# Optimization experiments

Measured on AMD Instinct MI355X. Metric: run time of the kernel, lower is better.

Reference implementation:

```python
import jax, jax.numpy as jnp
import numpy as np

H = 4096      # hidden_size (also vocab size of the embedding, per source)
O = 4096      # output_size (also embedding dim, per source)
MAX_LEN = 15


def setup_inputs() -> dict:
    key = jax.random.key(0)
    ks = jax.random.split(key, 16)
    s = 0.02  # init scale
    inp = {
        "input_ids": jax.random.randint(ks[0], (1,), 0, H),
        "hidden": jax.random.normal(ks[1], (1, 1, H), jnp.float32),
        "e_output": jax.random.normal(ks[2], (1, H), jnp.float32),   # unused, kept for signature fidelity
        "e_output_seq": jax.random.normal(ks[3], (MAX_LEN, H), jnp.float32),
        # parameters
        "emb_W": jax.random.normal(ks[4], (H, O), jnp.float32) * s,
        "att_W": jax.random.normal(ks[5], (MAX_LEN, H + O), jnp.float32) * s,
        "att_b": jnp.zeros((MAX_LEN,), jnp.float32),
        "comb_W": jax.random.normal(ks[6], (H, H + O), jnp.float32) * s,
        "comb_b": jnp.zeros((H,), jnp.float32),
        "gru_W_ih": jax.random.normal(ks[7], (3 * H, H), jnp.float32) * s,
        "gru_W_hh": jax.random.normal(ks[8], (3 * H, H), jnp.float32) * s,
        "gru_b_ih": jnp.zeros((3 * H,), jnp.float32),
        "gru_b_hh": jnp.zeros((3 * H,), jnp.float32),
        "out_W": jax.random.normal(ks[9], (O, H), jnp.float32) * s,
        "out_b": jnp.zeros((O,), jnp.float32),
    }
    return inp


def reference(input_ids, hidden, e_output, e_output_seq, emb_W, att_W, att_b,
              comb_W, comb_b, gru_W_ih, gru_W_hh, gru_b_ih, gru_b_hh, out_W, out_b):
    # dropout is identity in eval mode
    emb = emb_W[input_ids[0]][None, :]                       # [1, O]
    h0 = hidden[0]                                            # [1, H]
    att_logits = jnp.concatenate([emb, h0], axis=1) @ att_W.T + att_b
    att_weights = jax.nn.softmax(att_logits, axis=-1)         # [1, MAX_LEN]
    att_applied = att_weights @ e_output_seq                   # [1, H]
    combined = jnp.concatenate([emb, att_applied], axis=1)     # [1, H+O]
    x = jax.nn.relu(combined @ comb_W.T + comb_b)              # [1, H]
    # GRU cell (PyTorch gate order: r, z, n)
    gi = x @ gru_W_ih.T + gru_b_ih                             # [1, 3H]
    gh = h0 @ gru_W_hh.T + gru_b_hh                            # [1, 3H]
    i_r, i_z, i_n = jnp.split(gi, 3, axis=1)
    h_r, h_z, h_n = jnp.split(gh, 3, axis=1)
    r = jax.nn.sigmoid(i_r + h_r)
    z = jax.nn.sigmoid(i_z + h_z)
    n = jnp.tanh(i_n + r * h_n)
    h_new = (1.0 - z) * n + z * h0                             # [1, H]
    out = jax.nn.log_softmax(h_new @ out_W.T + out_b, axis=-1)  # [1, O]
    return out, h_new[None, :, :], att_weights
```

## Files before the change

### kernel.cpp

```cpp
#include <hip/hip_runtime.h>

#define H 4096
#define O 4096
#define HO 8192
#define MAXLEN 15

__device__ __forceinline__ float wave_dot(const float* __restrict__ w,
                                          const float* __restrict__ x,
                                          int K, int lane) {
    const float4* w4 = (const float4*)w;
    const float4* x4 = (const float4*)x;
    float acc = 0.f;
    int n4 = K >> 2;
    for (int i = lane; i < n4; i += 64) {
        float4 wv = w4[i];
        float4 xv = x4[i];
        acc += wv.x * xv.x + wv.y * xv.y + wv.z * xv.z + wv.w * xv.w;
    }
    #pragma unroll
    for (int off = 32; off; off >>= 1) acc += __shfl_down(acc, off, 64);
    return acc;
}

__global__ void k_att(const int* __restrict__ ids,
                      const float* __restrict__ hidden,
                      const float* __restrict__ eseq,
                      const float* __restrict__ embW,
                      const float* __restrict__ attW,
                      const float* __restrict__ attb,
                      float* __restrict__ combined,
                      float* __restrict__ out_attw) {
    __shared__ float s_logit[MAXLEN];
    __shared__ float s_w[MAXLEN];
    const int tid  = threadIdx.x;
    const int wave = tid >> 6, lane = tid & 63;
    const int id = ids[0];
    const float* emb = embW + (size_t)id * O;

    for (int k = tid; k < O; k += blockDim.x) combined[k] = emb[k];

    if (wave < MAXLEN) {
        const float* wrow = attW + (size_t)wave * (H + O);
        float acc = 0.f;
        for (int t = lane; t < O; t += 64) acc += emb[t] * wrow[t];
        for (int t = lane; t < H; t += 64) acc += hidden[t] * wrow[O + t];
        #pragma unroll
        for (int off = 32; off; off >>= 1) acc += __shfl_down(acc, off, 64);
        if (lane == 0) s_logit[wave] = acc + attb[wave];
    }
    __syncthreads();
    if (tid == 0) {
        float m = -1e30f;
        for (int j = 0; j < MAXLEN; j++) m = fmaxf(m, s_logit[j]);
        float s = 0.f;
        for (int j = 0; j < MAXLEN; j++) { float e = __expf(s_logit[j] - m); s_w[j] = e; s += e; }
        float inv = 1.f / s;
        for (int j = 0; j < MAXLEN; j++) { s_w[j] *= inv; out_attw[j] = s_w[j]; }
    }
    __syncthreads();
    for (int k = tid; k < H; k += blockDim.x) {
        float acc = 0.f;
        #pragma unroll
        for (int j = 0; j < MAXLEN; j++) acc += s_w[j] * eseq[j * H + k];
        combined[O + k] = acc;
    }
}

__global__ void k_comb_ghh(const float* __restrict__ combW,
                           const float* __restrict__ combB,
                           const float* __restrict__ ghhW,
                           const float* __restrict__ ghhB,
                           const float* __restrict__ hidden,
                           const float* __restrict__ combined,
                           float* __restrict__ xout,
                           float* __restrict__ ghout) {
    const int wave = threadIdx.x >> 6, lane = threadIdx.x & 63;
    const int b = blockIdx.x;
    if (b < 1024) {
        int row = b * 4 + wave;
        float d = wave_dot(combW + (size_t)row * HO, combined, HO, lane);
        if (lane == 0) xout[row] = fmaxf(d + combB[row], 0.f);
    } else {
        int row = (b - 1024) * 4 + wave;
        float d = wave_dot(ghhW + (size_t)row * H, hidden, H, lane);
        if (lane == 0) ghout[row] = d + ghhB[row];
    }
}

__global__ void k_gru(const float* __restrict__ gihW,
                      const float* __restrict__ gihB,
                      const float* __restrict__ hidden,
                      const float* __restrict__ x,
                      const float* __restrict__ gh,
                      float* __restrict__ hout,
                      float* __restrict__ out_h) {
    const int wave = threadIdx.x >> 6, lane = threadIdx.x & 63;
    const int i = blockIdx.x * 4 + wave;
    float d0 = wave_dot(gihW + (size_t)i * H,           x, H, lane);
    float d1 = wave_dot(gihW + (size_t)(i + H) * H,     x, H, lane);
    float d2 = wave_dot(gihW + (size_t)(i + 2 * H) * H, x, H, lane);
    if (lane == 0) {
        float ir = d0 + gihB[i];
        float iz = d1 + gihB[i + H];
        float in_ = d2 + gihB[i + 2 * H];
        float hr = gh[i], hz = gh[i + H], hn = gh[i + 2 * H];
        float r = 1.f / (1.f + __expf(-(ir + hr)));
        float z = 1.f / (1.f + __expf(-(iz + hz)));
        float n = tanhf(in_ + r * hn);
        float h0 = hidden[i];
        float h = (1.f - z) * n + z * h0;
        hout[i] = h;
        out_h[i] = h;
    }
}

__global__ void k_out(const float* __restrict__ outW,
                      const float* __restrict__ outB,
                      const float* __restrict__ h,
                      float* __restrict__ logits) {
    const int wave = threadIdx.x >> 6, lane = threadIdx.x & 63;
    const int i = blockIdx.x * 4 + wave;
    float d = wave_dot(outW + (size_t)i * H, h, H, lane);
    if (lane == 0) logits[i] = d + outB[i];
}

__global__ void k_lsm(const float* __restrict__ logits, float* __restrict__ out) {
    __shared__ float red[16];
    __shared__ float red2[16];
    const int tid = threadIdx.x, lane = tid & 63, wave = tid >> 6;
    float m = -1e30f;
    for (int k = tid; k < O; k += 1024) m = fmaxf(m, logits[k]);
    #pragma unroll
    for (int off = 32; off; off >>= 1) m = fmaxf(m, __shfl_down(m, off, 64));
    if (lane == 0) red[wave] = m;
    __syncthreads();
    if (tid == 0) {
        float mm = -1e30f;
        for (int j = 0; j < 16; j++) mm = fmaxf(mm, red[j]);
        red[0] = mm;
    }
    __syncthreads();
    m = red[0];
    float s = 0.f;
    for (int k = tid; k < O; k += 1024) s += __expf(logits[k] - m);
    #pragma unroll
    for (int off = 32; off; off >>= 1) s += __shfl_down(s, off, 64);
    if (lane == 0) red2[wave] = s;
    __syncthreads();
    if (tid == 0) {
        float ss = 0.f;
        for (int j = 0; j < 16; j++) ss += red2[j];
        red2[0] = m + logf(ss);
    }
    __syncthreads();
    float lse = red2[0];
    for (int k = tid; k < O; k += 1024) out[k] = logits[k] - lse;
}

extern "C" void kernel_launch(void* const* d_in, const int* in_sizes, int n_in,
                              void* d_out, int out_size, void* d_ws, size_t ws_size,
                              hipStream_t stream) {
    const int*   ids    = (const int*)d_in[0];
    const float* hidden = (const float*)d_in[1];
    const float* eseq   = (const float*)d_in[3];
    const float* embW   = (const float*)d_in[4];
    const float* attW   = (const float*)d_in[5];
    const float* attb   = (const float*)d_in[6];
    const float* combW  = (const float*)d_in[7];
    const float* combB  = (const float*)d_in[8];
    const float* gihW   = (const float*)d_in[9];
    const float* ghhW   = (const float*)d_in[10];
    const float* gihB   = (const float*)d_in[11];
    const float* ghhB   = (const float*)d_in[12];
    const float* outW   = (const float*)d_in[13];
    const float* outB   = (const float*)d_in[14];
    float* out = (float*)d_out;

    float* ws       = (float*)d_ws;
    float* combined = ws;
    float* xbuf     = ws + 8192;
    float* ghbuf    = ws + 12288;
    float* hbuf     = ws + 24576;
    float* logits   = ws + 28672;

    k_att     <<<1,    960,  0, stream>>>(ids, hidden, eseq, embW, attW, attb, combined, out + 8192);
    k_comb_ghh<<<4096, 256,  0, stream>>>(combW, combB, ghhW, ghhB, hidden, combined, xbuf, ghbuf);
    k_gru     <<<1024, 256,  0, stream>>>(gihW, gihB, hidden, xbuf, ghbuf, hbuf, out + 4096);
    k_out     <<<1024, 256,  0, stream>>>(outW, outB, hbuf, logits);
    k_lsm     <<<1,    1024, 0, stream>>>(logits, out);
}
```

Baseline: 614.4 us.

## Fuse decoder step into one persistent kernel with grid barriers

```diff
diff --git a/kernel.cpp b/kernel.cpp
--- a/kernel.cpp
+++ b/kernel.cpp
@@ -4,188 +4,229 @@
 #define O 4096
 #define HO 8192
 #define MAXLEN 15
-
-__device__ __forceinline__ float wave_dot(const float* __restrict__ w,
-                                          const float* __restrict__ x,
-                                          int K, int lane) {
-    const float4* w4 = (const float4*)w;
+#define NBLK 512
+
+struct Args {
+    const int* ids;
+    const float* hidden;
+    const float* eseq;
+    const float* embW;
+    const float* attW;
+    const float* attb;
+    const float* combW;
+    const float* combB;
+    const float* gihW;
+    const float* gihB;
+    const float* ghhW;
+    const float* ghhB;
+    const float* outW;
+    const float* outB;
+    float* out;
+    float* ws;
+};
+
+__device__ __forceinline__ float dot4f(const float4 a, const float4 b) {
+    return a.x * b.x + a.y * b.y + a.z * b.z + a.w * b.w;
+}
+
+#define XRED(v) { _Pragma("unroll") for (int o_ = 32; o_; o_ >>= 1) v += __shfl_xor(v, o_, 64); }
+
+__device__ __forceinline__ void loadx16(const float* __restrict__ x, int lane, float4 xs[16]) {
     const float4* x4 = (const float4*)x;
-    float acc = 0.f;
-    int n4 = K >> 2;
-    for (int i = lane; i < n4; i += 64) {
-        float4 wv = w4[i];
-        float4 xv = x4[i];
-        acc += wv.x * xv.x + wv.y * xv.y + wv.z * xv.z + wv.w * xv.w;
-    }
     #pragma unroll
-    for (int off = 32; off; off >>= 1) acc += __shfl_down(acc, off, 64);
-    return acc;
-}
-
-__global__ void k_att(const int* __restrict__ ids,
-                      const float* __restrict__ hidden,
-                      const float* __restrict__ eseq,
-                      const float* __restrict__ embW,
-                      const float* __restrict__ attW,
-                      const float* __restrict__ attb,
-                      float* __restrict__ combined,
-                      float* __restrict__ out_attw) {
-    __shared__ float s_logit[MAXLEN];
-    __shared__ float s_w[MAXLEN];
-    const int tid  = threadIdx.x;
-    const int wave = tid >> 6, lane = tid & 63;
-    const int id = ids[0];
-    const float* emb = embW + (size_t)id * O;
-
-    for (int k = tid; k < O; k += blockDim.x) combined[k] = emb[k];
-
-    if (wave < MAXLEN) {
-        const float* wrow = attW + (size_t)wave * (H + O);
-        float acc = 0.f;
-        for (int t = lane; t < O; t += 64) acc += emb[t] * wrow[t];
-        for (int t = lane; t < H; t += 64) acc += hidden[t] * wrow[O + t];
-        #pragma unroll
-        for (int off = 32; off; off >>= 1) acc += __shfl_down(acc, off, 64);
-        if (lane == 0) s_logit[wave] = acc + attb[wave];
-    }
+    for (int c = 0; c < 16; c++) xs[c] = x4[lane + c * 64];
+}
+
+__device__ __forceinline__ void dot16x2(const float* __restrict__ w0,
+                                        const float* __restrict__ w1,
+                                        const float4 xs[16], int lane,
+                                        float& s0, float& s1) {
+    const float4* a4 = (const float4*)w0;
+    const float4* b4 = (const float4*)w1;
+    float x0 = 0.f, x1 = 0.f;
+    #pragma unroll
+    for (int c = 0; c < 16; c++) {
+        x0 += dot4f(a4[lane + c * 64], xs[c]);
+        x1 += dot4f(b4[lane + c * 64], xs[c]);
+    }
+    s0 += x0; s1 += x1;
+}
+
+__device__ __forceinline__ void gsync(unsigned* ctr) {
     __syncthreads();
-    if (tid == 0) {
+    if (threadIdx.x == 0) {
+        __threadfence();
+        __hip_atomic_fetch_add(ctr, 1u, __ATOMIC_ACQ_REL, __HIP_MEMORY_SCOPE_AGENT);
+        while (__hip_atomic_load(ctr, __ATOMIC_ACQUIRE, __HIP_MEMORY_SCOPE_AGENT) < NBLK)
+            __builtin_amdgcn_s_sleep(2);
+        __threadfence();
+    }
+    __syncthreads();
+}
+
+__global__ void k_zero(unsigned* c) { if (threadIdx.x < 16) c[threadIdx.x] = 0; }
+
+__global__ __launch_bounds__(256, 2) void k_fused(Args a) {
+    __shared__ float red[4];
+    __shared__ float red2[4];
+    unsigned* ctr   = (unsigned*)a.ws;
+    float* combined = a.ws + 64;
+    float* xbuf     = a.ws + 64 + 8192;
+    float* hbuf     = a.ws + 64 + 12288;
+    float* logits   = a.ws + 64 + 16384;
+    float* attlog   = a.ws + 64 + 20480;
+
+    const int tid = threadIdx.x, lane = tid & 63, w4 = tid >> 6;
+    const int gw = blockIdx.x * 4 + w4;
+    const int i0 = gw, i1 = gw + 2048;
+
+    float hr0, hz0, hn0, hr1, hz1, hn1;
+    {
+        float4 hs[16];
+        loadx16(a.hidden, lane, hs);
+        float s00 = 0.f, s10 = 0.f, s01 = 0.f, s11 = 0.f, s02 = 0.f, s12 = 0.f;
+        dot16x2(a.ghhW + (size_t)i0 * H,           a.ghhW + (size_t)i1 * H,           hs, lane, s00, s10);
+        dot16x2(a.ghhW + (size_t)(i0 + H) * H,     a.ghhW + (size_t)(i1 + H) * H,     hs, lane, s01, s11);
+        dot16x2(a.ghhW + (size_t)(i0 + 2 * H) * H, a.ghhW + (size_t)(i1 + 2 * H) * H, hs, lane, s02, s12);
+        XRED(s00); XRED(s10); XRED(s01); XRED(s11); XRED(s02); XRED(s12);
+        hr0 = s00 + a.ghhB[i0]; hz0 = s01 + a.ghhB[i0 + H]; hn0 = s02 + a.ghhB[i0 + 2 * H];
+        hr1 = s10 + a.ghhB[i1]; hz1 = s11 + a.ghhB[i1 + H]; hn1 = s12 + a.ghhB[i1 + 2 * H];
+
+        if (gw < MAXLEN) {
+            const int id = a.ids[0];
+            const float* ar = a.attW + (size_t)gw * HO;
+            float4 es[16];
+            loadx16(a.embW + (size_t)id * O, lane, es);
+            float sa = 0.f, sb = 0.f;
+            dot16x2(ar, ar + O, es, lane, sa, sb);
+            sb = 0.f;
+            {
+                const float4* b4 = (const float4*)(ar + O);
+                #pragma unroll
+                for (int c = 0; c < 16; c++) sb += dot4f(b4[lane + c * 64], hs[c]);
+            }
+            float s = sa + sb;
+            XRED(s);
+            if (lane == 0) attlog[gw] = s + a.attb[gw];
+        }
+    }
+    gsync(ctr + 0);
+
+    if (blockIdx.x < 32) {
+        const int k = blockIdx.x * 256 + tid;
+        float l[MAXLEN];
         float m = -1e30f;
-        for (int j = 0; j < MAXLEN; j++) m = fmaxf(m, s_logit[j]);
+        #pragma unroll
+        for (int j = 0; j < MAXLEN; j++) { l[j] = attlog[j]; m = fmaxf(m, l[j]); }
         float s = 0.f;
-        for (int j = 0; j < MAXLEN; j++) { float e = __expf(s_logit[j] - m); s_w[j] = e; s += e; }
-        float inv = 1.f / s;
-        for (int j = 0; j < MAXLEN; j++) { s_w[j] *= inv; out_attw[j] = s_w[j]; }
-    }
-    __syncthreads();
-    for (int k = tid; k < H; k += blockDim.x) {
-        float acc = 0.f;
-        #pragma unroll
-        for (int j = 0; j < MAXLEN; j++) acc += s_w[j] * eseq[j * H + k];
-        combined[O + k] = acc;
-    }
-}
-
-__global__ void k_comb_ghh(const float* __restrict__ combW,
-                           const float* __restrict__ combB,
-                           const float* __restrict__ ghhW,
-                           const float* __restrict__ ghhB,
-                           const float* __restrict__ hidden,
-                           const float* __restrict__ combined,
-                           float* __restrict__ xout,
-                           float* __restrict__ ghout) {
-    const int wave = threadIdx.x >> 6, lane = threadIdx.x & 63;
-    const int b = blockIdx.x;
-    if (b < 1024) {
-        int row = b * 4 + wave;
-        float d = wave_dot(combW + (size_t)row * HO, combined, HO, lane);
-        if (lane == 0) xout[row] = fmaxf(d + combB[row], 0.f);
-    } else {
-        int row = (b - 1024) * 4 + wave;
-        float d = wave_dot(ghhW + (size_t)row * H, hidden, H, lane);
-        if (lane == 0) ghout[row] = d + ghhB[row];
-    }
-}
-
-__global__ void k_gru(const float* __restrict__ gihW,
-                      const float* __restrict__ gihB,
-                      const float* __restrict__ hidden,
-                      const float* __restrict__ x,
-                      const float* __restrict__ gh,
-                      float* __restrict__ hout,
-                      float* __restrict__ out_h) {
-    const int wave = threadIdx.x >> 6, lane = threadIdx.x & 63;
-    const int i = blockIdx.x * 4 + wave;
-    float d0 = wave_dot(gihW + (size_t)i * H,           x, H, lane);
-    float d1 = wave_dot(gihW + (size_t)(i + H) * H,     x, H, lane);
-    float d2 = wave_dot(gihW + (size_t)(i + 2 * H) * H, x, H, lane);
-    if (lane == 0) {
-        float ir = d0 + gihB[i];
-        float iz = d1 + gihB[i + H];
-        float in_ = d2 + gihB[i + 2 * H];
-        float hr = gh[i], hz = gh[i + H], hn = gh[i + 2 * H];
-        float r = 1.f / (1.f + __expf(-(ir + hr)));
-        float z = 1.f / (1.f + __expf(-(iz + hz)));
-        float n = tanhf(in_ + r * hn);
-        float h0 = hidden[i];
-        float h = (1.f - z) * n + z * h0;
-        hout[i] = h;
-        out_h[i] = h;
-    }
-}
-
-__global__ void k_out(const float* __restrict__ outW,
-                      const float* __restrict__ outB,
-                      const float* __restrict__ h,
-                      float* __restrict__ logits) {
-    const int wave = threadIdx.x >> 6, lane = threadIdx.x & 63;
-    const int i = blockIdx.x * 4 + wave;
-    float d = wave_dot(outW + (size_t)i * H, h, H, lane);
-    if (lane == 0) logits[i] = d + outB[i];
-}
-
-__global__ void k_lsm(const float* __restrict__ logits, float* __restrict__ out) {
-    __shared__ float red[16];
-    __shared__ float red2[16];
-    const int tid = threadIdx.x, lane = tid & 63, wave = tid >> 6;
-    float m = -1e30f;
-    for (int k = tid; k < O; k += 1024) m = fmaxf(m, logits[k]);
-    #pragma unroll
-    for (int off = 32; off; off >>= 1) m = fmaxf(m, __shfl_down(m, off, 64));
-    if (lane == 0) red[wave] = m;
-    __syncthreads();
-    if (tid == 0) {
-        float mm = -1e30f;
-        for (int j = 0; j < 16; j++) mm = fmaxf(mm, red[j]);
-        red[0] = mm;
-    }
-    __syncthreads();
-    m = red[0];
-    float s = 0.f;
-    for (int k = tid; k < O; k += 1024) s += __expf(logits[k] - m);
-    #pragma unroll
-    for (int off = 32; off; off >>= 1) s += __shfl_down(s, off, 64);
-    if (lane == 0) red2[wave] = s;
-    __syncthreads();
-    if (tid == 0) {
-        float ss = 0.f;
-        for (int j = 0; j < 16; j++) ss += red2[j];
-        red2[0] = m + logf(ss);
-    }
-    __syncthreads();
-    float lse = red2[0];
-    for (int k = tid; k < O; k += 1024) out[k] = logits[k] - lse;
+        #pragma unroll
+        for (int j = 0; j < MAXLEN; j++) { l[j] = __expf(l[j] - m); s += l[j]; }
+        const float inv = 1.f / s;
+        if (k < O) {
+            combined[k] = a.embW[(size_t)a.ids[0] * O + k];
+            if (k < MAXLEN) a.out[8192 + k] = l[k] * inv;
+        } else {
+            const int kk = k - O;
+            float acc = 0.f;
+            #pragma unroll
+            for (int j = 0; j < MAXLEN; j++) acc += l[j] * a.eseq[j * H + kk];
+            combined[k] = acc * inv;
+        }
+    }
+    gsync(ctr + 1);
+
+    {
+        float s0 = 0.f, s1 = 0.f;
+        #pragma unroll
+        for (int hh = 0; hh < 2; hh++) {
+            float4 xs[16];
+            loadx16(combined + hh * 4096, lane, xs);
+            dot16x2(a.combW + (size_t)i0 * HO + hh * 4096,
+                    a.combW + (size_t)i1 * HO + hh * 4096, xs, lane, s0, s1);
+        }
+        XRED(s0); XRED(s1);
+        if (lane == 0) {
+            xbuf[i0] = fmaxf(s0 + a.combB[i0], 0.f);
+            xbuf[i1] = fmaxf(s1 + a.combB[i1], 0.f);
+        }
+    }
+    gsync(ctr + 2);
+
+    {
+        float4 xs[16];
+        loadx16(xbuf, lane, xs);
+        float s00 = 0.f, s10 = 0.f, s01 = 0.f, s11 = 0.f, s02 = 0.f, s12 = 0.f;
+        dot16x2(a.gihW + (size_t)i0 * H,           a.gihW + (size_t)i1 * H,           xs, lane, s00, s10);
+        dot16x2(a.gihW + (size_t)(i0 + H) * H,     a.gihW + (size_t)(i1 + H) * H,     xs, lane, s01, s11);
+        dot16x2(a.gihW + (size_t)(i0 + 2 * H) * H, a.gihW + (size_t)(i1 + 2 * H) * H, xs, lane, s02, s12);
+        XRED(s00); XRED(s10); XRED(s01); XRED(s11); XRED(s02); XRED(s12);
+        if (lane == 0) {
+            float r0 = 1.f / (1.f + __expf(-(s00 + a.gihB[i0] + hr0)));
+            float z0 = 1.f / (1.f + __expf(-(s01 + a.gihB[i0 + H] + hz0)));
+            float n0 = tanhf(s02 + a.gihB[i0 + 2 * H] + r0 * hn0);
+            float h0 = (1.f - z0) * n0 + z0 * a.hidden[i0];
+            hbuf[i0] = h0; a.out[4096 + i0] = h0;
+            float r1 = 1.f / (1.f + __expf(-(s10 + a.gihB[i1] + hr1)));
+            float z1 = 1.f / (1.f + __expf(-(s11 + a.gihB[i1 + H] + hz1)));
+            float n1 = tanhf(s12 + a.gihB[i1 + 2 * H] + r1 * hn1);
+            float h1 = (1.f - z1) * n1 + z1 * a.hidden[i1];
+            hbuf[i1] = h1; a.out[4096 + i1] = h1;
+        }
+    }
+    gsync(ctr + 3);
+
+    {
+        float4 xs[16];
+        loadx16(hbuf, lane, xs);
+        float s0 = 0.f, s1 = 0.f;
+        dot16x2(a.outW + (size_t)i0 * H, a.outW + (size_t)i1 * H, xs, lane, s0, s1);
+        XRED(s0); XRED(s1);
+        if (lane == 0) {
+            logits[i0] = s0 + a.outB[i0];
+            logits[i1] = s1 + a.outB[i1];
+        }
+    }
+    gsync(ctr + 4);
+
+    if (blockIdx.x == 0) {
+        float m = -1e30f;
+        for (int k = tid; k < O; k += 256) m = fmaxf(m, logits[k]);
+        #pragma unroll
+        for (int o_ = 32; o_; o_ >>= 1) m = fmaxf(m, __shfl_xor(m, o_, 64));
+        if (lane == 0) red[w4] = m;
+        __syncthreads();
+        m = fmaxf(fmaxf(red[0], red[1]), fmaxf(red[2], red[3]));
+        float s = 0.f;
+        for (int k = tid; k < O; k += 256) s += __expf(logits[k] - m);
+        XRED(s);
+        if (lane == 0) red2[w4] = s;
+        __syncthreads();
+        const float lse = m + logf(red2[0] + red2[1] + red2[2] + red2[3]);
+        for (int k = tid; k < O; k += 256) a.out[k] = logits[k] - lse;
+    }
 }
 
 extern "C" void kernel_launch(void* const* d_in, const int* in_sizes, int n_in,
                               void* d_out, int out_size, void* d_ws, size_t ws_size,
                               hipStream_t stream) {
-    const int*   ids    = (const int*)d_in[0];
-    const float* hidden = (const float*)d_in[1];
-    const float* eseq   = (const float*)d_in[3];
-    const float* embW   = (const float*)d_in[4];
-    const float* attW   = (const float*)d_in[5];
-    const float* attb   = (const float*)d_in[6];
-    const float* combW  = (const float*)d_in[7];
-    const float* combB  = (const float*)d_in[8];
-    const float* gihW   = (const float*)d_in[9];
-    const float* ghhW   = (const float*)d_in[10];
-    const float* gihB   = (const float*)d_in[11];
-    const float* ghhB   = (const float*)d_in[12];
-    const float* outW   = (const float*)d_in[13];
-    const float* outB   = (const float*)d_in[14];
-    float* out = (float*)d_out;
-
-    float* ws       = (float*)d_ws;
-    float* combined = ws;
-    float* xbuf     = ws + 8192;
-    float* ghbuf    = ws + 12288;
-    float* hbuf     = ws + 24576;
-    float* logits   = ws + 28672;
-
-    k_att     <<<1,    960,  0, stream>>>(ids, hidden, eseq, embW, attW, attb, combined, out + 8192);
-    k_comb_ghh<<<4096, 256,  0, stream>>>(combW, combB, ghhW, ghhB, hidden, combined, xbuf, ghbuf);
-    k_gru     <<<1024, 256,  0, stream>>>(gihW, gihB, hidden, xbuf, ghbuf, hbuf, out + 4096);
-    k_out     <<<1024, 256,  0, stream>>>(outW, outB, hbuf, logits);
-    k_lsm     <<<1,    1024, 0, stream>>>(logits, out);
-}
+    Args a;
+    a.ids    = (const int*)d_in[0];
+    a.hidden = (const float*)d_in[1];
+    a.eseq   = (const float*)d_in[3];
+    a.embW   = (const float*)d_in[4];
+    a.attW   = (const float*)d_in[5];
+    a.attb   = (const float*)d_in[6];
+    a.combW  = (const float*)d_in[7];
+    a.combB  = (const float*)d_in[8];
+    a.gihW   = (const float*)d_in[9];
+    a.ghhW   = (const float*)d_in[10];
+    a.gihB   = (const float*)d_in[11];
+    a.ghhB   = (const float*)d_in[12];
+    a.outW   = (const float*)d_in[13];
+    a.outB   = (const float*)d_in[14];
+    a.out    = (float*)d_out;
+    a.ws     = (float*)d_ws;
+
+    k_zero<<<1, 64, 0, stream>>>((unsigned*)d_ws);
+    k_fused<<<NBLK, 256, 0, stream>>>(a);
+}
```

Result: slower. 959.8 us (+56.2%).
